# Kernel optimization log

Hardware: AMD Instinct MI355X
Metric: run time of the kernel (lower is better)

Reference implementation:

```python
import jax, jax.numpy as jnp
import numpy as np

VOCAB = 32000
D_MODEL = 192
N_LAYERS = 8
D_STATE = 64
EXPAND = 2
D_CONV = 3
NUM_CLASSES = 2
D_INNER = EXPAND * D_MODEL            # 384
DT_RANK = (D_MODEL + 15) // 16        # 12 (mamba_ssm default ceil(d_model/16))
EPS = 1e-6


def rmsnorm(x, w):
    return w * x * jax.lax.rsqrt(jnp.mean(x * x, axis=-1, keepdims=True) + EPS)


def selective_scan(u, dt, A, Bm, Cm):
    # u, dt: (b, T, d_inner); Bm, Cm: (b, T, d_state); A: (d_inner, d_state)
    def step(h, xs):
        dt_t, B_t, C_t, u_t = xs                      # (b,di),(b,ds),(b,ds),(b,di)
        dA = jnp.exp(dt_t[:, :, None] * A)            # (b, di, ds)
        h = dA * h + (dt_t * u_t)[:, :, None] * B_t[:, None, :]
        y = jnp.einsum('bdn,bn->bd', h, C_t)
        return h, y

    b = u.shape[0]
    h0 = jnp.zeros((b, D_INNER, D_STATE), u.dtype)
    xs = (jnp.swapaxes(dt, 0, 1), jnp.swapaxes(Bm, 0, 1),
          jnp.swapaxes(Cm, 0, 1), jnp.swapaxes(u, 0, 1))
    _, ys = jax.lax.scan(step, h0, xs)                # ys: (T, b, di)
    return jnp.swapaxes(ys, 0, 1)


def mamba_layer(x, p):
    # one residual Mamba block: x + Mamba(RMSNorm(x))
    norm_w, in_w, cw, cb, xpw, dtw, dtb, Alog, Dp, ow = p
    h = rmsnorm(x, norm_w)
    xz = jnp.einsum('btd,ed->bte', h, in_w)           # (b, T, 2*di)
    xi, z = jnp.split(xz, 2, axis=-1)
    # causal depthwise conv over time
    xc = jnp.swapaxes(xi, 1, 2)                       # (b, di, T)
    xc = jax.lax.conv_general_dilated(xc, cw[:, None, :], (1,),
                                      [(D_CONV - 1, 0)],
                                      feature_group_count=D_INNER)
    xi = jax.nn.silu(jnp.swapaxes(xc, 1, 2) + cb)
    dbl = jnp.einsum('btc,ec->bte', xi, xpw)          # (b, T, dt_rank+2*ds)
    dt_r = dbl[..., :DT_RANK]
    Bm = dbl[..., DT_RANK:DT_RANK + D_STATE]
    Cm = dbl[..., DT_RANK + D_STATE:]
    dt = jax.nn.softplus(jnp.einsum('btr,dr->btd', dt_r, dtw) + dtb)
    A = -jnp.exp(Alog)
    y = selective_scan(xi, dt, A, Bm, Cm) + xi * Dp
    y = y * jax.nn.silu(z)
    return x + jnp.einsum('bte,de->btd', y, ow)


def setup_inputs():
    key = jax.random.key(0)
    ks = jax.random.split(key, 12)
    B, L = 8, 1024
    s = 0.02
    input_ids = jax.random.randint(ks[0], (B, L), 0, VOCAB, dtype=jnp.int32)
    attention_mask = jnp.ones((B, L), dtype=jnp.int32)
    embed = jax.random.normal(ks[1], (VOCAB, D_MODEL), jnp.float32) * s
    cls = jax.random.normal(ks[2], (1, 1, D_MODEL), jnp.float32) * s
    norm_w = jnp.ones((N_LAYERS, D_MODEL), jnp.float32)
    in_proj_w = jax.random.normal(ks[3], (N_LAYERS, 2 * D_INNER, D_MODEL), jnp.float32) * s
    conv_w = jax.random.normal(ks[4], (N_LAYERS, D_INNER, D_CONV), jnp.float32) * s
    conv_b = jnp.zeros((N_LAYERS, D_INNER), jnp.float32)
    x_proj_w = jax.random.normal(ks[5], (N_LAYERS, DT_RANK + 2 * D_STATE, D_INNER), jnp.float32) * s
    dt_proj_w = jax.random.normal(ks[6], (N_LAYERS, D_INNER, DT_RANK), jnp.float32) * s
    dt_proj_b = jnp.zeros((N_LAYERS, D_INNER), jnp.float32)
    # mamba_ssm S4D-real init: A_log = log(1..d_state)
    A_log = jnp.log(jnp.tile(jnp.arange(1.0, D_STATE + 1, dtype=jnp.float32)[None, None, :],
                             (N_LAYERS, D_INNER, 1)))
    D_param = jnp.ones((N_LAYERS, D_INNER), jnp.float32)
    out_proj_w = jax.random.normal(ks[7], (N_LAYERS, D_MODEL, D_INNER), jnp.float32) * s
    final_norm_w = jnp.ones((D_MODEL,), jnp.float32)
    head_w = embed[:NUM_CLASSES]            # tie_embeddings=True
    head_b = jnp.zeros((NUM_CLASSES,), jnp.float32)
    return dict(input_ids=input_ids, attention_mask=attention_mask, embed=embed,
                cls=cls, norm_w=norm_w, in_proj_w=in_proj_w, conv_w=conv_w,
                conv_b=conv_b, x_proj_w=x_proj_w, dt_proj_w=dt_proj_w,
                dt_proj_b=dt_proj_b, A_log=A_log, D_param=D_param,
                out_proj_w=out_proj_w, final_norm_w=final_norm_w,
                head_w=head_w, head_b=head_b)


def reference(input_ids, attention_mask, embed, cls, norm_w, in_proj_w, conv_w,
              conv_b, x_proj_w, dt_proj_w, dt_proj_b, A_log, D_param,
              out_proj_w, final_norm_w, head_w, head_b):
    x = embed[input_ids]                               # (b, L, d)
    b = x.shape[0]
    x = jnp.concatenate([x, jnp.broadcast_to(cls, (b, 1, D_MODEL))], axis=1)
    layer_fn = jax.checkpoint(mamba_layer)

    def body(x, p):
        return layer_fn(x, p), None

    x, _ = jax.lax.scan(body, x, (norm_w, in_proj_w, conv_w, conv_b, x_proj_w,
                                  dt_proj_w, dt_proj_b, A_log, D_param, out_proj_w))
    x = rmsnorm(x, final_norm_w)
    m = attention_mask.astype(x.dtype)                 # (b, L)
    denom = jnp.clip(jnp.sum(m, axis=1, keepdims=True), 1.0, None)
    pooled = jnp.sum(x[:, :-1] * m[..., None], axis=1) / denom
    return pooled @ head_w.T + head_b                  # (b, num_classes)
```

## Files before the change

### kernel.cpp

```cpp
#include <hip/hip_runtime.h>
#include <hip/hip_bf16.h>
#include <cstddef>

namespace {

constexpr int NB   = 8;
constexpr int LSEQ = 1025;
constexpr int TSEQ = 1024;
constexpr int DM   = 192;
constexpr int DI   = 384;
constexpr int DXZ  = 768;
constexpr int DBLW = 140;
constexpr int DTR  = 12;
constexpr int NST  = 64;
constexpr int MROWS = NB * LSEQ;
constexpr int NCH  = 64;
constexpr int CS   = 16;
constexpr int NCH1 = NCH - 1;
constexpr int NDG  = DI / 64;
constexpr int HST  = 32;
constexpr int XPAD = 144;
constexpr float LOG2E = 1.4426950408889634f;

using bf16x8 = __attribute__((ext_vector_type(8))) short;
using f32x4  = __attribute__((ext_vector_type(4))) float;

__device__ __forceinline__ float waveReduceSum(float v) {
#pragma unroll
  for (int o = 32; o; o >>= 1) v += __shfl_xor(v, o, 64);
  return v;
}

__device__ __forceinline__ unsigned short f2bf(float v) {
  __hip_bfloat16 b = __float2bfloat16(v);
  return *reinterpret_cast<unsigned short*>(&b);
}
__device__ __forceinline__ float bf2f(unsigned short u) {
  return __uint_as_float(((unsigned)u) << 16);
}
__device__ __forceinline__ unsigned addpair_bf(unsigned a, unsigned b) {
  float alo = __uint_as_float(a << 16), ahi = __uint_as_float(a & 0xffff0000u);
  float blo = __uint_as_float(b << 16), bhi = __uint_as_float(b & 0xffff0000u);
  return ((unsigned)f2bf(alo + blo)) | (((unsigned)f2bf(ahi + bhi)) << 16);
}

__global__ void embed_kernel(const int* __restrict__ ids, const float* __restrict__ emb,
                             const float* __restrict__ cls, float* __restrict__ x) {
  int idx = blockIdx.x * blockDim.x + threadIdx.x;
  if (idx >= NB * LSEQ * DM) return;
  int d = idx % DM;
  int bt = idx / DM;
  int t = bt % LSEQ, b = bt / LSEQ;
  float v;
  if (t < TSEQ) v = emb[(size_t)ids[b * TSEQ + t] * DM + d];
  else          v = cls[d];
  x[idx] = v;
}

__global__ void cvt_bf16_kernel(const float* __restrict__ src, unsigned short* __restrict__ dst,
                                int n) {
  int idx = blockIdx.x * blockDim.x + threadIdx.x;
  if (idx < n) dst[idx] = f2bf(src[idx]);
}

__global__ void pad_xp_kernel(const float* __restrict__ src, unsigned short* __restrict__ dst) {
  int idx = blockIdx.x * blockDim.x + threadIdx.x;
  if (idx >= 8 * XPAD * DI) return;
  int k = idx % DI;
  int n = (idx / DI) % XPAD;
  int l = idx / (DI * XPAD);
  float v = (n < DBLW) ? src[((size_t)l * DBLW + n) * DI + k] : 0.f;
  dst[idx] = f2bf(v);
}

__global__ void transpose_batched(const float* __restrict__ in, float* __restrict__ out,
                                  int rows, int cols) {
  __shared__ float tile[32][33];
  int l = blockIdx.z;
  int r0 = blockIdx.y * 32, c0 = blockIdx.x * 32;
  const float* src = in + (size_t)l * rows * cols;
  float* dst = out + (size_t)l * rows * cols;
  int tx = threadIdx.x, ty = threadIdx.y;
#pragma unroll
  for (int i = 0; i < 32; i += 8) {
    int r = r0 + ty + i, c = c0 + tx;
    if (r < rows && c < cols) tile[ty + i][tx] = src[(size_t)r * cols + c];
  }
  __syncthreads();
#pragma unroll
  for (int i = 0; i < 32; i += 8) {
    int c = c0 + ty + i, r = r0 + tx;
    if (c < cols && r < rows) dst[(size_t)c * rows + r] = tile[tx][ty + i];
  }
}

__global__ __launch_bounds__(192)
void rmsnorm_kernel(const float* __restrict__ x, const float* __restrict__ w,
                    unsigned short* __restrict__ h) {
  int row = blockIdx.x;
  int d = threadIdx.x;
  float v = x[(size_t)row * DM + d];
  float ss = waveReduceSum(v * v);
  __shared__ float red[3];
  if ((d & 63) == 0) red[d >> 6] = ss;
  __syncthreads();
  float ms = (red[0] + red[1] + red[2]) * (1.f / DM);
  h[(size_t)row * DM + d] = f2bf(v * rsqrtf(ms + 1e-6f) * w[d]);
}

template <int EPI, int ASRC>
__global__ __launch_bounds__(256)
void gemm_mfma(const unsigned short* __restrict__ A, const unsigned short* __restrict__ Ab0,
               const unsigned short* __restrict__ Ab1, const unsigned short* __restrict__ W,
               float* __restrict__ C, unsigned short* __restrict__ Cb,
               int M, int Nw, int Nstore, int K, int ldc) {
  __shared__ unsigned short Alds[128][40];
  __shared__ unsigned short Wlds[64][40];
  const int tid = threadIdx.x;
  const int w = tid >> 6, lane = tid & 63;
  const int r16 = lane & 15, g = lane >> 4;
  const int row0 = blockIdx.y * 128, col0 = blockIdx.x * 64;

  f32x4 acc[2][4];
#pragma unroll
  for (int mi = 0; mi < 2; ++mi)
#pragma unroll
    for (int ni = 0; ni < 4; ++ni) acc[mi][ni] = (f32x4){0.f, 0.f, 0.f, 0.f};

  for (int k0 = 0; k0 < K; k0 += 32) {
#pragma unroll
    for (int cc = 0; cc < 2; ++cc) {
      int c = tid + cc * 256;
      int r = c >> 2, q = c & 3;
      uint4 v = make_uint4(0, 0, 0, 0);
      int grow = row0 + r;
      if (grow < M) {
        if (ASRC == 0) {
          v = *(const uint4*)(A + (size_t)grow * K + k0 + q * 8);
        } else {
          uint4 a = *(const uint4*)(Ab0 + (size_t)grow * K + k0 + q * 8);
          uint4 b = *(const uint4*)(Ab1 + (size_t)grow * K + k0 + q * 8);
          v.x = addpair_bf(a.x, b.x);
          v.y = addpair_bf(a.y, b.y);
          v.z = addpair_bf(a.z, b.z);
          v.w = addpair_bf(a.w, b.w);
        }
      }
      *(uint4*)&Alds[r][q * 8] = v;
    }
    {
      int r = tid >> 2, q = tid & 3;
      uint4 v = make_uint4(0, 0, 0, 0);
      int gn = col0 + r;
      if (gn < Nw) v = *(const uint4*)(W + (size_t)gn * K + k0 + q * 8);
      *(uint4*)&Wlds[r][q * 8] = v;
    }
    __syncthreads();
    bf16x8 a_f[2], b_f[4];
#pragma unroll
    for (int mi = 0; mi < 2; ++mi)
      a_f[mi] = *(const bf16x8*)&Alds[w * 32 + mi * 16 + r16][g * 8];
#pragma unroll
    for (int ni = 0; ni < 4; ++ni)
      b_f[ni] = *(const bf16x8*)&Wlds[ni * 16 + r16][g * 8];
#pragma unroll
    for (int mi = 0; mi < 2; ++mi)
#pragma unroll
      for (int ni = 0; ni < 4; ++ni)
        acc[mi][ni] = __builtin_amdgcn_mfma_f32_16x16x32_bf16(a_f[mi], b_f[ni],
                                                              acc[mi][ni], 0, 0, 0);
    __syncthreads();
  }
#pragma unroll
  for (int mi = 0; mi < 2; ++mi) {
#pragma unroll
    for (int reg = 0; reg < 4; ++reg) {
      int row = row0 + w * 32 + mi * 16 + g * 4 + reg;
      if (row >= M) continue;
#pragma unroll
      for (int ni = 0; ni < 4; ++ni) {
        int col = col0 + ni * 16 + r16;
        if (col >= Nstore) continue;
        size_t idx = (size_t)row * ldc + col;
        if (EPI == 1)      C[idx] += acc[mi][ni][reg];
        else if (EPI == 0) C[idx] = acc[mi][ni][reg];
        else               Cb[idx] = f2bf(acc[mi][ni][reg]);
      }
    }
  }
}

__global__ void conv_kernel(const unsigned short* __restrict__ xz16, const float* __restrict__ cw,
                            const float* __restrict__ cb,
                            unsigned short* __restrict__ xi16,
                            unsigned short* __restrict__ zg16) {
  int idx = blockIdx.x * blockDim.x + threadIdx.x;
  if (idx >= NB * LSEQ * DI) return;
  int c = idx % DI;
  int bt = idx / DI;
  int t = bt % LSEQ, b = bt / LSEQ;
  const unsigned short* src = xz16 + (size_t)b * LSEQ * DXZ + c;
  float s = cb[c];
  float w0 = cw[c * 3 + 0], w1 = cw[c * 3 + 1], w2 = cw[c * 3 + 2];
  if (t >= 2) s = fmaf(w0, bf2f(src[(size_t)(t - 2) * DXZ]), s);
  if (t >= 1) s = fmaf(w1, bf2f(src[(size_t)(t - 1) * DXZ]), s);
  s = fmaf(w2, bf2f(src[(size_t)t * DXZ]), s);
  float sig = 1.f / (1.f + __expf(-s));
  float u = s * sig;
  xi16[idx] = f2bf(u);
  float zv = bf2f(src[(size_t)t * DXZ + DI]);
  float zsig = 1.f / (1.f + __expf(-zv));
  zg16[idx] = f2bf(zv * zsig);
}

__global__ __launch_bounds__(384)
void dt_kernel(const float* __restrict__ dbl, const float* __restrict__ dtwT,
               const float* __restrict__ dtb, float* __restrict__ dtout) {
  int row0 = blockIdx.x * 4;
  int d = threadIdx.x;
  __shared__ float rr[4][DTR];
  if (d < 4 * DTR) rr[d / DTR][d % DTR] = dbl[(size_t)(row0 + d / DTR) * DBLW + (d % DTR)];
  float w[DTR];
#pragma unroll
  for (int r = 0; r < DTR; ++r) w[r] = dtwT[r * DI + d];
  float bias = dtb[d];
  __syncthreads();
#pragma unroll
  for (int q = 0; q < 4; ++q) {
    float s = bias;
#pragma unroll
    for (int r = 0; r < DTR; ++r) s = fmaf(rr[q][r], w[r], s);
    float sp = fmaxf(s, 0.f) + log1pf(__expf(-fabsf(s)));
    dtout[(size_t)(row0 + q) * DI + d] = sp;
  }
}


__global__ __launch_bounds__(768, 6)
void scan_pass1(const float* __restrict__ dtp_, const unsigned short* __restrict__ xi16,
                const float* __restrict__ dbl, const float* __restrict__ Alog,
                float* __restrict__ cumdt, float* __restrict__ H) {
  __shared__ float Bt[CS][64];
  const int tid = threadIdx.x;
  const int w = tid >> 6, lane = tid & 63;
  const int dgrp = w >> 1, half = w & 1;
  const int b = blockIdx.x / NCH1;
  const int c = blockIdx.x % NCH1;
  const int bg = b * NDG + dgrp;
  const int d = dgrp * 64 + lane;
  const int n0 = half * HST;
  const int t0 = c * CS;

  {
    const float* srcB = dbl + ((size_t)b * LSEQ + t0) * DBLW + DTR + lane;
    for (int r = w; r < CS; r += 12) Bt[r][lane] = srcB[(size_t)r * DBLW];
  }

  const float* Ap = Alog + (size_t)d * NST;
  float a0 = __expf(Ap[0]);
  bool okl = true;
#pragma unroll
  for (int j = 0; j < HST; ++j) {
    float aj = __expf(Ap[n0 + j]);
    okl = okl && (fabsf(aj - (float)(n0 + j + 1) * a0) <= 1e-3f * (float)(n0 + j + 1) * fabsf(a0));
  }
  const bool fast = __all(okl);
  const float al2u = -a0 * LOG2E;

  float h[HST];
#pragma unroll
  for (int j = 0; j < HST; ++j) h[j] = 0.f;

  __syncthreads();

  const float* dtp = dtp_ + ((size_t)b * LSEQ + t0) * DI + d;
  const unsigned short* up = xi16 + ((size_t)b * LSEQ + t0) * DI + d;
  float cum = 0.f;
  float dtv = *dtp, uv = bf2f(*up);

  if (fast) {
    for (int t = 0; t < CS; ++t) {
      float n_dt = 0.f, n_u = 0.f;
      if (t + 1 < CS) {
        dtp += DI; up += DI;
        n_dt = *dtp; n_u = bf2f(*up);
      }
      float dtu = dtv * uv;
      float m = dtv * al2u;
      float r1 = exp2f(m);
      float p = (n0 == 0) ? r1 : exp2f(m * (float)(n0 + 1));
      float r2 = r1 * r1, r4 = r2 * r2;
      float s0 = p, s1 = p * r1, s2 = p * r2, s3 = s2 * r1;
#pragma unroll
      for (int k = 0; k < 8; ++k) {
        float4 B4 = *(const float4*)&Bt[t][n0 + 4 * k];
        h[4 * k + 0] = fmaf(s0, h[4 * k + 0], dtu * B4.x);
        h[4 * k + 1] = fmaf(s1, h[4 * k + 1], dtu * B4.y);
        h[4 * k + 2] = fmaf(s2, h[4 * k + 2], dtu * B4.z);
        h[4 * k + 3] = fmaf(s3, h[4 * k + 3], dtu * B4.w);
        if (k < 7) { s0 *= r4; s1 *= r4; s2 *= r4; s3 *= r4; }
      }
      cum += dtv;
      dtv = n_dt; uv = n_u;
    }
  } else {
    for (int t = 0; t < CS; ++t) {
      float n_dt = 0.f, n_u = 0.f;
      if (t + 1 < CS) {
        dtp += DI; up += DI;
        n_dt = *dtp; n_u = bf2f(*up);
      }
      float dtu = dtv * uv;
      for (int j = 0; j < HST; ++j) {
        float aj = -__expf(Ap[n0 + j]) * LOG2E;
        h[j] = fmaf(exp2f(dtv * aj), h[j], dtu * Bt[t][n0 + j]);
      }
      cum += dtv;
      dtv = n_dt; uv = n_u;
    }
  }

  if (half == 0)
    cumdt[(size_t)bg * NCH1 * 64 + (size_t)c * 64 + lane] = cum;
  float* hp = H + ((size_t)bg * NCH + (c + 1)) * NST * 64 + (size_t)n0 * 64 + lane;
#pragma unroll
  for (int j = 0; j < HST; ++j) hp[j * 64] = h[j];
}

__global__ __launch_bounds__(256)
void scan_pass2(const float* __restrict__ cumdt, const float* __restrict__ Alog,
                float* __restrict__ H) {
  int gw = blockIdx.x * 4 + (threadIdx.x >> 6);
  int lane = threadIdx.x & 63;
  int bg = gw >> 4;
  int nq = (gw & 15) * 4;
  int dgrp = bg % NDG;
  int d = dgrp * 64 + lane;

  float al2[4];
#pragma unroll
  for (int j = 0; j < 4; ++j) al2[j] = -__expf(Alog[(size_t)d * NST + nq + j]) * LOG2E;

  float h[4] = {0.f, 0.f, 0.f, 0.f};

  float* H0 = H + ((size_t)bg * NCH) * NST * 64 + (size_t)nq * 64 + lane;
#pragma unroll
  for (int j = 0; j < 4; ++j) H0[j * 64] = 0.f;

  for (int c = 1; c < NCH; ++c) {
    float cum = cumdt[(size_t)bg * NCH1 * 64 + (size_t)(c - 1) * 64 + lane];
    float* Hc = H + ((size_t)bg * NCH + c) * NST * 64 + (size_t)nq * 64 + lane;
#pragma unroll
    for (int j = 0; j < 4; ++j) {
      float he = Hc[j * 64];
      h[j] = fmaf(exp2f(al2[j] * cum), h[j], he);
      Hc[j * 64] = h[j];
    }
  }
}

__global__ __launch_bounds__(768, 6)
void scan_pass3(const float* __restrict__ dtp_, const unsigned short* __restrict__ xi16,
                const unsigned short* __restrict__ zg16, const float* __restrict__ dbl,
                const float* __restrict__ Alog, const float* __restrict__ Dpar,
                const float* __restrict__ H, unsigned short* __restrict__ yb0,
                unsigned short* __restrict__ yb1) {
  __shared__ float Bt[CS + 1][64];
  __shared__ float Ct[CS + 1][64];
  const int tid = threadIdx.x;
  const int w = tid >> 6, lane = tid & 63;
  const int dgrp = w >> 1, half = w & 1;
  const int b = blockIdx.x >> 6;
  const int c = blockIdx.x & 63;
  const int bg = b * NDG + dgrp;
  const int d = dgrp * 64 + lane;
  const int n0 = half * HST;
  const int t0 = c * CS;
  const int nsteps = (c == NCH - 1) ? (LSEQ - t0) : CS;

  {
    if (w < 6) {
      const float* srcB = dbl + ((size_t)b * LSEQ + t0) * DBLW + DTR + lane;
      for (int r = w; r < nsteps; r += 6) Bt[r][lane] = srcB[(size_t)r * DBLW];
    } else {
      const float* srcC = dbl + ((size_t)b * LSEQ + t0) * DBLW + DTR + NST + lane;
      for (int r = w - 6; r < nsteps; r += 6) Ct[r][lane] = srcC[(size_t)r * DBLW];
    }
  }

  const float* Ap = Alog + (size_t)d * NST;
  float a0 = __expf(Ap[0]);
  bool okl = true;
#pragma unroll
  for (int j = 0; j < HST; ++j) {
    float aj = __expf(Ap[n0 + j]);
    okl = okl && (fabsf(aj - (float)(n0 + j + 1) * a0) <= 1e-3f * (float)(n0 + j + 1) * fabsf(a0));
  }
  const bool fast = __all(okl);
  const float al2u = -a0 * LOG2E;

  float Dp = Dpar[d];
  float h[HST];
  {
    const float* hi = H + ((size_t)bg * NCH + c) * NST * 64 + (size_t)n0 * 64 + lane;
#pragma unroll
    for (int j = 0; j < HST; ++j) h[j] = hi[j * 64];
  }

  __syncthreads();

  const float* dtp = dtp_ + ((size_t)b * LSEQ + t0) * DI + d;
  const unsigned short* up = xi16 + ((size_t)b * LSEQ + t0) * DI + d;
  const unsigned short* gp = zg16 + ((size_t)b * LSEQ + t0) * DI + d;
  unsigned short* yp = (half == 0 ? yb0 : yb1) + ((size_t)b * LSEQ + t0) * DI + d;

  float dtv = *dtp, uv = bf2f(*up), gv = bf2f(*gp);

  if (fast) {
    for (int t = 0; t < nsteps; ++t) {
      float n_dt = 0.f, n_u = 0.f, n_g = 0.f;
      if (t + 1 < nsteps) {
        dtp += DI; up += DI; gp += DI;
        n_dt = *dtp; n_u = bf2f(*up); n_g = bf2f(*gp);
      }
      float dtu = dtv * uv;
      float m = dtv * al2u;
      float r1 = exp2f(m);
      float p = (n0 == 0) ? r1 : exp2f(m * (float)(n0 + 1));
      float r2 = r1 * r1, r4 = r2 * r2;
      float s0 = p, s1 = p * r1, s2 = p * r2, s3 = s2 * r1;
      float y = 0.f;
#pragma unroll
      for (int k = 0; k < 8; ++k) {
        float4 B4 = *(const float4*)&Bt[t][n0 + 4 * k];
        float4 C4 = *(const float4*)&Ct[t][n0 + 4 * k];
        h[4 * k + 0] = fmaf(s0, h[4 * k + 0], dtu * B4.x);
        y = fmaf(h[4 * k + 0], C4.x, y);
        h[4 * k + 1] = fmaf(s1, h[4 * k + 1], dtu * B4.y);
        y = fmaf(h[4 * k + 1], C4.y, y);
        h[4 * k + 2] = fmaf(s2, h[4 * k + 2], dtu * B4.z);
        y = fmaf(h[4 * k + 2], C4.z, y);
        h[4 * k + 3] = fmaf(s3, h[4 * k + 3], dtu * B4.w);
        y = fmaf(h[4 * k + 3], C4.w, y);
        if (k < 7) { s0 *= r4; s1 *= r4; s2 *= r4; s3 *= r4; }
      }
      float outv = (half == 0) ? fmaf(uv, Dp, y) * gv : y * gv;
      *yp = f2bf(outv);
      yp += DI;
      dtv = n_dt; uv = n_u; gv = n_g;
    }
  } else {
    for (int t = 0; t < nsteps; ++t) {
      float n_dt = 0.f, n_u = 0.f, n_g = 0.f;
      if (t + 1 < nsteps) {
        dtp += DI; up += DI; gp += DI;
        n_dt = *dtp; n_u = bf2f(*up); n_g = bf2f(*gp);
      }
      float dtu = dtv * uv;
      float y = 0.f;
      for (int j = 0; j < HST; ++j) {
        float aj = -__expf(Ap[n0 + j]) * LOG2E;
        h[j] = fmaf(exp2f(dtv * aj), h[j], dtu * Bt[t][n0 + j]);
        y = fmaf(h[j], Ct[t][n0 + j], y);
      }
      float outv = (half == 0) ? fmaf(uv, Dp, y) * gv : y * gv;
      *yp = f2bf(outv);
      yp += DI;
      dtv = n_dt; uv = n_u; gv = n_g;
    }
  }
}

__global__ __launch_bounds__(192)
void pool1_kernel(const float* __restrict__ x, const int* __restrict__ mask,
                  const float* __restrict__ fw, float* __restrict__ partial) {
  int b = blockIdx.x >> 6;
  int chunk = blockIdx.x & 63;
  int d = threadIdx.x;
  __shared__ float red[3];
  float w = fw[d];
  float acc = 0.f;
  for (int tt = 0; tt < 16; ++tt) {
    int t = chunk * 16 + tt;
    float v = x[((size_t)b * LSEQ + t) * DM + d];
    float ss = waveReduceSum(v * v);
    if ((d & 63) == 0) red[d >> 6] = ss;
    __syncthreads();
    float ms = (red[0] + red[1] + red[2]) * (1.f / DM);
    float m = (float)mask[b * TSEQ + t];
    acc = fmaf(v * rsqrtf(ms + 1e-6f) * w, m, acc);
    __syncthreads();
  }
  partial[((size_t)b * 64 + chunk) * DM + d] = acc;
}

__global__ __launch_bounds__(192)
void pool2_kernel(const float* __restrict__ partial, const int* __restrict__ mask,
                  const float* __restrict__ hw, const float* __restrict__ hb,
                  float* __restrict__ out) {
  int b = blockIdx.x;
  int d = threadIdx.x;
  float s = 0.f;
  for (int c = 0; c < 64; ++c) s += partial[((size_t)b * 64 + c) * DM + d];
  float den = 0.f;
  for (int t = d; t < TSEQ; t += DM) den += (float)mask[b * TSEQ + t];
  den = waveReduceSum(den);
  __shared__ float dred[3];
  __shared__ float pooled[DM];
  if ((d & 63) == 0) dred[d >> 6] = den;
  __syncthreads();
  float denom = fmaxf(dred[0] + dred[1] + dred[2], 1.f);
  pooled[d] = s / denom;
  __syncthreads();
  if (d < 2) {
    float acc = hb[d];
    for (int k = 0; k < DM; ++k) acc = fmaf(pooled[k], hw[d * DM + k], acc);
    out[b * 2 + d] = acc;
  }
}

}

extern "C" void kernel_launch(void* const* d_in, const int* in_sizes, int n_in,
                              void* d_out, int out_size, void* d_ws, size_t ws_size,
                              hipStream_t stream) {
  const int*   ids    = (const int*)d_in[0];
  const int*   mask   = (const int*)d_in[1];
  const float* embed  = (const float*)d_in[2];
  const float* cls    = (const float*)d_in[3];
  const float* norm_w = (const float*)d_in[4];
  const float* in_w   = (const float*)d_in[5];
  const float* conv_w = (const float*)d_in[6];
  const float* conv_b = (const float*)d_in[7];
  const float* xp_w   = (const float*)d_in[8];
  const float* dtw    = (const float*)d_in[9];
  const float* dtb    = (const float*)d_in[10];
  const float* Alog   = (const float*)d_in[11];
  const float* Dpar   = (const float*)d_in[12];
  const float* ow     = (const float*)d_in[13];
  const float* fnw    = (const float*)d_in[14];
  const float* hw     = (const float*)d_in[15];
  const float* hb     = (const float*)d_in[16];
  float* out = (float*)d_out;

  char* base = (char*)d_ws;
  size_t off = 0;
  auto alloc = [&](size_t bytes) -> void* {
    void* p = base + off;
    off = (off + bytes + 255) & ~(size_t)255;
    return p;
  };

  float* x      = (float*)alloc((size_t)NB * LSEQ * DM * 4);
  unsigned short* h16 = (unsigned short*)alloc((size_t)NB * LSEQ * DM * 2);
  unsigned short* xz16 = (unsigned short*)alloc((size_t)NB * LSEQ * DXZ * 2);
  unsigned short* xi16 = (unsigned short*)alloc((size_t)NB * LSEQ * DI * 2);
  unsigned short* zg16 = (unsigned short*)alloc((size_t)NB * LSEQ * DI * 2);
  float* dblb   = (float*)alloc((size_t)NB * LSEQ * DBLW * 4);
  float* dtbuf  = (float*)alloc((size_t)NB * LSEQ * DI * 4);
  unsigned short* yb0 = (unsigned short*)alloc((size_t)NB * LSEQ * DI * 2);
  unsigned short* yb1 = (unsigned short*)alloc((size_t)NB * LSEQ * DI * 2);
  unsigned short* wb_in = (unsigned short*)alloc((size_t)8 * DXZ * DM * 2);
  unsigned short* wb_xp = (unsigned short*)alloc((size_t)8 * XPAD * DI * 2);
  unsigned short* wb_ow = (unsigned short*)alloc((size_t)8 * DM * DI * 2);
  float* wT_dt  = (float*)alloc((size_t)8 * DTR * DI * 4);
  float* partial = (float*)alloc((size_t)NB * 64 * DM * 4);
  float* cumdt  = (float*)alloc((size_t)NB * NDG * NCH1 * 64 * 4);
  float* Hbuf   = (float*)alloc((size_t)NB * NDG * NCH * NST * 64 * 4);

  cvt_bf16_kernel<<<(8 * DXZ * DM + 255) / 256, 256, 0, stream>>>(in_w, wb_in, 8 * DXZ * DM);
  pad_xp_kernel<<<(8 * XPAD * DI + 255) / 256, 256, 0, stream>>>(xp_w, wb_xp);
  cvt_bf16_kernel<<<(8 * DM * DI + 255) / 256, 256, 0, stream>>>(ow, wb_ow, 8 * DM * DI);
  dim3 tb(32, 8);
  transpose_batched<<<dim3(1, 12, 8), tb, 0, stream>>>(dtw, wT_dt, DI, DTR);

  embed_kernel<<<(NB * LSEQ * DM) / 256, 256, 0, stream>>>(ids, embed, cls, x);

  const int mtiles = (MROWS + 127) / 128;
  for (int l = 0; l < 8; ++l) {
    rmsnorm_kernel<<<MROWS, 192, 0, stream>>>(x, norm_w + l * DM, h16);
    gemm_mfma<2, 0><<<dim3(DXZ / 64, mtiles), 256, 0, stream>>>(
        h16, nullptr, nullptr, wb_in + (size_t)l * DXZ * DM, nullptr, xz16,
        MROWS, DXZ, DXZ, DM, DXZ);
    conv_kernel<<<(NB * LSEQ * DI) / 256, 256, 0, stream>>>(
        xz16, conv_w + l * DI * 3, conv_b + l * DI, xi16, zg16);
    gemm_mfma<0, 0><<<dim3(XPAD / 64 + 1, mtiles), 256, 0, stream>>>(
        xi16, nullptr, nullptr, wb_xp + (size_t)l * XPAD * DI, dblb, nullptr,
        MROWS, XPAD, DBLW, DI, DBLW);
    dt_kernel<<<MROWS / 4, DI, 0, stream>>>(dblb, wT_dt + l * DTR * DI, dtb + l * DI, dtbuf);
    scan_pass1<<<NB * NCH1, 768, 0, stream>>>(
        dtbuf, xi16, dblb, Alog + (size_t)l * DI * NST, cumdt, Hbuf);
    scan_pass2<<<(NB * NDG * 16) / 4, 256, 0, stream>>>(
        cumdt, Alog + (size_t)l * DI * NST, Hbuf);
    scan_pass3<<<NB * NCH, 768, 0, stream>>>(
        dtbuf, xi16, zg16, dblb, Alog + (size_t)l * DI * NST, Dpar + l * DI, Hbuf,
        yb0, yb1);
    gemm_mfma<1, 1><<<dim3(DM / 64, mtiles), 256, 0, stream>>>(
        nullptr, yb0, yb1, wb_ow + (size_t)l * DM * DI, x, nullptr,
        MROWS, DM, DM, DI, DM);
  }

  pool1_kernel<<<NB * 64, 192, 0, stream>>>(x, mask, fnw, partial);
  pool2_kernel<<<NB, 192, 0, stream>>>(partial, mask, hw, hb, out);
}
```

Baseline: 1.391 ms.

## Split scan state into quarters with longer chunks and four partial-y buffers

Changes the chunked selective scan from 64 chunks of 16 steps with two state-halves per d-group to 32 chunks of 32 steps. Each wave now owns a quarter of the state (16 registers), and each block covers half of the d-groups. Four partial y buffers are written and then summed inside the out-projection GEMM's A-load. The aim is lower register pressure per thread and less inter-chunk H traffic in pass2, with more parallel lanes per step. The cost is extra y-buffer memory traffic, four loads per A element in the GEMM, and longer serial chunks.

```diff
diff --git a/kernel.cpp b/kernel.cpp
--- a/kernel.cpp
+++ b/kernel.cpp
@@ -14,11 +14,11 @@
 constexpr int DTR  = 12;
 constexpr int NST  = 64;
 constexpr int MROWS = NB * LSEQ;
-constexpr int NCH  = 64;
-constexpr int CS   = 16;
+constexpr int NCH  = 32;
+constexpr int CS   = 32;
 constexpr int NCH1 = NCH - 1;
 constexpr int NDG  = DI / 64;
-constexpr int HST  = 32;
+constexpr int HST  = 16;
 constexpr int XPAD = 144;
 constexpr float LOG2E = 1.4426950408889634f;
 
@@ -111,7 +111,8 @@
 template <int EPI, int ASRC>
 __global__ __launch_bounds__(256)
 void gemm_mfma(const unsigned short* __restrict__ A, const unsigned short* __restrict__ Ab0,
-               const unsigned short* __restrict__ Ab1, const unsigned short* __restrict__ W,
+               const unsigned short* __restrict__ Ab1, const unsigned short* __restrict__ Ab2,
+               const unsigned short* __restrict__ Ab3, const unsigned short* __restrict__ W,
                float* __restrict__ C, unsigned short* __restrict__ Cb,
                int M, int Nw, int Nstore, int K, int ldc) {
   __shared__ unsigned short Alds[128][40];
@@ -140,10 +141,12 @@
         } else {
           uint4 a = *(const uint4*)(Ab0 + (size_t)grow * K + k0 + q * 8);
           uint4 b = *(const uint4*)(Ab1 + (size_t)grow * K + k0 + q * 8);
-          v.x = addpair_bf(a.x, b.x);
-          v.y = addpair_bf(a.y, b.y);
-          v.z = addpair_bf(a.z, b.z);
-          v.w = addpair_bf(a.w, b.w);
+          uint4 cq = *(const uint4*)(Ab2 + (size_t)grow * K + k0 + q * 8);
+          uint4 dq = *(const uint4*)(Ab3 + (size_t)grow * K + k0 + q * 8);
+          v.x = addpair_bf(addpair_bf(a.x, b.x), addpair_bf(cq.x, dq.x));
+          v.y = addpair_bf(addpair_bf(a.y, b.y), addpair_bf(cq.y, dq.y));
+          v.z = addpair_bf(addpair_bf(a.z, b.z), addpair_bf(cq.z, dq.z));
+          v.w = addpair_bf(addpair_bf(a.w, b.w), addpair_bf(cq.w, dq.w));
         }
       }
       *(uint4*)&Alds[r][q * 8] = v;
@@ -243,12 +246,14 @@
   __shared__ float Bt[CS][64];
   const int tid = threadIdx.x;
   const int w = tid >> 6, lane = tid & 63;
-  const int dgrp = w >> 1, half = w & 1;
-  const int b = blockIdx.x / NCH1;
-  const int c = blockIdx.x % NCH1;
+  const int dgrp_l = w >> 2, quarter = w & 3;
+  const int b = blockIdx.x / (NCH1 * 2);
+  const int rem = blockIdx.x % (NCH1 * 2);
+  const int c = rem >> 1, hb = rem & 1;
+  const int dgrp = hb * 3 + dgrp_l;
   const int bg = b * NDG + dgrp;
   const int d = dgrp * 64 + lane;
-  const int n0 = half * HST;
+  const int n0 = quarter * HST;
   const int t0 = c * CS;
 
   {
@@ -288,17 +293,17 @@
       float dtu = dtv * uv;
       float m = dtv * al2u;
       float r1 = exp2f(m);
-      float p = (n0 == 0) ? r1 : exp2f(m * (float)(n0 + 1));
+      float p = (quarter == 0) ? r1 : exp2f(m * (float)(n0 + 1));
       float r2 = r1 * r1, r4 = r2 * r2;
       float s0 = p, s1 = p * r1, s2 = p * r2, s3 = s2 * r1;
 #pragma unroll
-      for (int k = 0; k < 8; ++k) {
+      for (int k = 0; k < HST / 4; ++k) {
         float4 B4 = *(const float4*)&Bt[t][n0 + 4 * k];
         h[4 * k + 0] = fmaf(s0, h[4 * k + 0], dtu * B4.x);
         h[4 * k + 1] = fmaf(s1, h[4 * k + 1], dtu * B4.y);
         h[4 * k + 2] = fmaf(s2, h[4 * k + 2], dtu * B4.z);
         h[4 * k + 3] = fmaf(s3, h[4 * k + 3], dtu * B4.w);
-        if (k < 7) { s0 *= r4; s1 *= r4; s2 *= r4; s3 *= r4; }
+        if (k < HST / 4 - 1) { s0 *= r4; s1 *= r4; s2 *= r4; s3 *= r4; }
       }
       cum += dtv;
       dtv = n_dt; uv = n_u;
@@ -320,7 +325,7 @@
     }
   }
 
-  if (half == 0)
+  if (quarter == 0)
     cumdt[(size_t)bg * NCH1 * 64 + (size_t)c * 64 + lane] = cum;
   float* hp = H + ((size_t)bg * NCH + (c + 1)) * NST * 64 + (size_t)n0 * 64 + lane;
 #pragma unroll
@@ -363,18 +368,21 @@
 void scan_pass3(const float* __restrict__ dtp_, const unsigned short* __restrict__ xi16,
                 const unsigned short* __restrict__ zg16, const float* __restrict__ dbl,
                 const float* __restrict__ Alog, const float* __restrict__ Dpar,
-                const float* __restrict__ H, unsigned short* __restrict__ yb0,
-                unsigned short* __restrict__ yb1) {
+                const float* __restrict__ H,
+                unsigned short* __restrict__ yq0, unsigned short* __restrict__ yq1,
+                unsigned short* __restrict__ yq2, unsigned short* __restrict__ yq3) {
   __shared__ float Bt[CS + 1][64];
   __shared__ float Ct[CS + 1][64];
   const int tid = threadIdx.x;
   const int w = tid >> 6, lane = tid & 63;
-  const int dgrp = w >> 1, half = w & 1;
+  const int dgrp_l = w >> 2, quarter = w & 3;
   const int b = blockIdx.x >> 6;
-  const int c = blockIdx.x & 63;
+  const int rem = blockIdx.x & 63;
+  const int c = rem >> 1, hb = rem & 1;
+  const int dgrp = hb * 3 + dgrp_l;
   const int bg = b * NDG + dgrp;
   const int d = dgrp * 64 + lane;
-  const int n0 = half * HST;
+  const int n0 = quarter * HST;
   const int t0 = c * CS;
   const int nsteps = (c == NCH - 1) ? (LSEQ - t0) : CS;
 
@@ -412,7 +420,8 @@
   const float* dtp = dtp_ + ((size_t)b * LSEQ + t0) * DI + d;
   const unsigned short* up = xi16 + ((size_t)b * LSEQ + t0) * DI + d;
   const unsigned short* gp = zg16 + ((size_t)b * LSEQ + t0) * DI + d;
-  unsigned short* yp = (half == 0 ? yb0 : yb1) + ((size_t)b * LSEQ + t0) * DI + d;
+  unsigned short* yp = (quarter == 0 ? yq0 : quarter == 1 ? yq1 : quarter == 2 ? yq2 : yq3)
+                       + ((size_t)b * LSEQ + t0) * DI + d;
 
   float dtv = *dtp, uv = bf2f(*up), gv = bf2f(*gp);
 
@@ -426,12 +435,12 @@
       float dtu = dtv * uv;
       float m = dtv * al2u;
       float r1 = exp2f(m);
-      float p = (n0 == 0) ? r1 : exp2f(m * (float)(n0 + 1));
+      float p = (quarter == 0) ? r1 : exp2f(m * (float)(n0 + 1));
       float r2 = r1 * r1, r4 = r2 * r2;
       float s0 = p, s1 = p * r1, s2 = p * r2, s3 = s2 * r1;
       float y = 0.f;
 #pragma unroll
-      for (int k = 0; k < 8; ++k) {
+      for (int k = 0; k < HST / 4; ++k) {
         float4 B4 = *(const float4*)&Bt[t][n0 + 4 * k];
         float4 C4 = *(const float4*)&Ct[t][n0 + 4 * k];
         h[4 * k + 0] = fmaf(s0, h[4 * k + 0], dtu * B4.x);
@@ -442,9 +451,9 @@
         y = fmaf(h[4 * k + 2], C4.z, y);
         h[4 * k + 3] = fmaf(s3, h[4 * k + 3], dtu * B4.w);
         y = fmaf(h[4 * k + 3], C4.w, y);
-        if (k < 7) { s0 *= r4; s1 *= r4; s2 *= r4; s3 *= r4; }
-      }
-      float outv = (half == 0) ? fmaf(uv, Dp, y) * gv : y * gv;
+        if (k < HST / 4 - 1) { s0 *= r4; s1 *= r4; s2 *= r4; s3 *= r4; }
+      }
+      float outv = (quarter == 0) ? fmaf(uv, Dp, y) * gv : y * gv;
       *yp = f2bf(outv);
       yp += DI;
       dtv = n_dt; uv = n_u; gv = n_g;
@@ -463,7 +472,7 @@
         h[j] = fmaf(exp2f(dtv * aj), h[j], dtu * Bt[t][n0 + j]);
         y = fmaf(h[j], Ct[t][n0 + j], y);
       }
-      float outv = (half == 0) ? fmaf(uv, Dp, y) * gv : y * gv;
+      float outv = (quarter == 0) ? fmaf(uv, Dp, y) * gv : y * gv;
       *yp = f2bf(outv);
       yp += DI;
       dtv = n_dt; uv = n_u; gv = n_g;
@@ -558,8 +567,10 @@
   unsigned short* zg16 = (unsigned short*)alloc((size_t)NB * LSEQ * DI * 2);
   float* dblb   = (float*)alloc((size_t)NB * LSEQ * DBLW * 4);
   float* dtbuf  = (float*)alloc((size_t)NB * LSEQ * DI * 4);
-  unsigned short* yb0 = (unsigned short*)alloc((size_t)NB * LSEQ * DI * 2);
-  unsigned short* yb1 = (unsigned short*)alloc((size_t)NB * LSEQ * DI * 2);
+  unsigned short* yq0 = (unsigned short*)alloc((size_t)NB * LSEQ * DI * 2);
+  unsigned short* yq1 = (unsigned short*)alloc((size_t)NB * LSEQ * DI * 2);
+  unsigned short* yq2 = (unsigned short*)alloc((size_t)NB * LSEQ * DI * 2);
+  unsigned short* yq3 = (unsigned short*)alloc((size_t)NB * LSEQ * DI * 2);
   unsigned short* wb_in = (unsigned short*)alloc((size_t)8 * DXZ * DM * 2);
   unsigned short* wb_xp = (unsigned short*)alloc((size_t)8 * XPAD * DI * 2);
   unsigned short* wb_ow = (unsigned short*)alloc((size_t)8 * DM * DI * 2);
@@ -580,24 +591,24 @@
   for (int l = 0; l < 8; ++l) {
     rmsnorm_kernel<<<MROWS, 192, 0, stream>>>(x, norm_w + l * DM, h16);
     gemm_mfma<2, 0><<<dim3(DXZ / 64, mtiles), 256, 0, stream>>>(
-        h16, nullptr, nullptr, wb_in + (size_t)l * DXZ * DM, nullptr, xz16,
-        MROWS, DXZ, DXZ, DM, DXZ);
+        h16, nullptr, nullptr, nullptr, nullptr, wb_in + (size_t)l * DXZ * DM,
+        nullptr, xz16, MROWS, DXZ, DXZ, DM, DXZ);
     conv_kernel<<<(NB * LSEQ * DI) / 256, 256, 0, stream>>>(
         xz16, conv_w + l * DI * 3, conv_b + l * DI, xi16, zg16);
     gemm_mfma<0, 0><<<dim3(XPAD / 64 + 1, mtiles), 256, 0, stream>>>(
-        xi16, nullptr, nullptr, wb_xp + (size_t)l * XPAD * DI, dblb, nullptr,
-        MROWS, XPAD, DBLW, DI, DBLW);
+        xi16, nullptr, nullptr, nullptr, nullptr, wb_xp + (size_t)l * XPAD * DI,
+        dblb, nullptr, MROWS, XPAD, DBLW, DI, DBLW);
     dt_kernel<<<MROWS / 4, DI, 0, stream>>>(dblb, wT_dt + l * DTR * DI, dtb + l * DI, dtbuf);
-    scan_pass1<<<NB * NCH1, 768, 0, stream>>>(
+    scan_pass1<<<NB * NCH1 * 2, 768, 0, stream>>>(
         dtbuf, xi16, dblb, Alog + (size_t)l * DI * NST, cumdt, Hbuf);
     scan_pass2<<<(NB * NDG * 16) / 4, 256, 0, stream>>>(
         cumdt, Alog + (size_t)l * DI * NST, Hbuf);
-    scan_pass3<<<NB * NCH, 768, 0, stream>>>(
+    scan_pass3<<<NB * NCH * 2, 768, 0, stream>>>(
         dtbuf, xi16, zg16, dblb, Alog + (size_t)l * DI * NST, Dpar + l * DI, Hbuf,
-        yb0, yb1);
+        yq0, yq1, yq2, yq3);
     gemm_mfma<1, 1><<<dim3(DM / 64, mtiles), 256, 0, stream>>>(
-        nullptr, yb0, yb1, wb_ow + (size_t)l * DM * DI, x, nullptr,
-        MROWS, DM, DM, DI, DM);
+        nullptr, yq0, yq1, yq2, yq3, wb_ow + (size_t)l * DM * DI,
+        x, nullptr, MROWS, DM, DM, DI, DM);
   }
 
   pool1_kernel<<<NB * 64, 192, 0, stream>>>(x, mask, fnw, partial);
```

After: 1.319 ms. -5.1%, faster.

## Restructure chunked scan: scalar B/C loads, bf16 chunk states, larger chunks

Applied to the files above, without the earlier changes.

The chunked selective scan now uses 32-step chunks instead of 16, which halves the number of chunk states. Blocks shrink from 768 to 128 threads, each handling one 64-channel group. B and C are no longer staged in shared memory; they are read through wave-uniform (readfirstlane) pointers so they can go through scalar loads, which also removes the __syncthreads. Inter-chunk states H are stored in bf16 instead of fp32 to halve that traffic, and the y reduction is split into four accumulators for more ILP. The bf16 state storage loses precision across the chunk carry, and longer chunks lengthen the serial part of each block.

```diff
diff --git a/kernel.cpp b/kernel.cpp
--- a/kernel.cpp
+++ b/kernel.cpp
@@ -14,8 +14,8 @@
 constexpr int DTR  = 12;
 constexpr int NST  = 64;
 constexpr int MROWS = NB * LSEQ;
-constexpr int NCH  = 64;
-constexpr int CS   = 16;
+constexpr int NCH  = 32;
+constexpr int CS   = 32;
 constexpr int NCH1 = NCH - 1;
 constexpr int NDG  = DI / 64;
 constexpr int HST  = 32;
@@ -42,6 +42,12 @@
   float alo = __uint_as_float(a << 16), ahi = __uint_as_float(a & 0xffff0000u);
   float blo = __uint_as_float(b << 16), bhi = __uint_as_float(b & 0xffff0000u);
   return ((unsigned)f2bf(alo + blo)) | (((unsigned)f2bf(ahi + bhi)) << 16);
+}
+__device__ __forceinline__ const float* uniform_ptr(const float* p) {
+  unsigned long long v = (unsigned long long)p;
+  unsigned lo = __builtin_amdgcn_readfirstlane((unsigned)v);
+  unsigned hi = __builtin_amdgcn_readfirstlane((unsigned)(v >> 32));
+  return (const float*)(((unsigned long long)hi << 32) | lo);
 }
 
 __global__ void embed_kernel(const int* __restrict__ ids, const float* __restrict__ emb,
@@ -236,25 +242,23 @@
 }
 
 
-__global__ __launch_bounds__(768, 6)
+__global__ __launch_bounds__(128, 4)
 void scan_pass1(const float* __restrict__ dtp_, const unsigned short* __restrict__ xi16,
                 const float* __restrict__ dbl, const float* __restrict__ Alog,
-                float* __restrict__ cumdt, float* __restrict__ H) {
-  __shared__ float Bt[CS][64];
+                float* __restrict__ cumdt, unsigned short* __restrict__ H) {
   const int tid = threadIdx.x;
-  const int w = tid >> 6, lane = tid & 63;
-  const int dgrp = w >> 1, half = w & 1;
-  const int b = blockIdx.x / NCH1;
-  const int c = blockIdx.x % NCH1;
+  const int half = tid >> 6, lane = tid & 63;
+  const int b = blockIdx.x / (NCH1 * NDG);
+  const int rem = blockIdx.x % (NCH1 * NDG);
+  const int c = rem / NDG;
+  const int dgrp = rem % NDG;
   const int bg = b * NDG + dgrp;
   const int d = dgrp * 64 + lane;
   const int n0 = half * HST;
   const int t0 = c * CS;
 
-  {
-    const float* srcB = dbl + ((size_t)b * LSEQ + t0) * DBLW + DTR + lane;
-    for (int r = w; r < CS; r += 12) Bt[r][lane] = srcB[(size_t)r * DBLW];
-  }
+  const int n0u = __builtin_amdgcn_readfirstlane(n0);
+  const float* Bg = uniform_ptr(dbl + ((size_t)b * LSEQ + t0) * DBLW + DTR + n0u);
 
   const float* Ap = Alog + (size_t)d * NST;
   float a0 = __expf(Ap[0]);
@@ -270,8 +274,6 @@
   float h[HST];
 #pragma unroll
   for (int j = 0; j < HST; ++j) h[j] = 0.f;
-
-  __syncthreads();
 
   const float* dtp = dtp_ + ((size_t)b * LSEQ + t0) * DI + d;
   const unsigned short* up = xi16 + ((size_t)b * LSEQ + t0) * DI + d;
@@ -288,12 +290,13 @@
       float dtu = dtv * uv;
       float m = dtv * al2u;
       float r1 = exp2f(m);
-      float p = (n0 == 0) ? r1 : exp2f(m * (float)(n0 + 1));
+      float p = (n0u == 0) ? r1 : exp2f(m * (float)(n0u + 1));
       float r2 = r1 * r1, r4 = r2 * r2;
       float s0 = p, s1 = p * r1, s2 = p * r2, s3 = s2 * r1;
+      const float* Bu = Bg + (size_t)t * DBLW;
 #pragma unroll
       for (int k = 0; k < 8; ++k) {
-        float4 B4 = *(const float4*)&Bt[t][n0 + 4 * k];
+        float4 B4 = *(const float4*)(Bu + 4 * k);
         h[4 * k + 0] = fmaf(s0, h[4 * k + 0], dtu * B4.x);
         h[4 * k + 1] = fmaf(s1, h[4 * k + 1], dtu * B4.y);
         h[4 * k + 2] = fmaf(s2, h[4 * k + 2], dtu * B4.z);
@@ -311,9 +314,10 @@
         n_dt = *dtp; n_u = bf2f(*up);
       }
       float dtu = dtv * uv;
+      const float* Bu = Bg + (size_t)t * DBLW;
       for (int j = 0; j < HST; ++j) {
         float aj = -__expf(Ap[n0 + j]) * LOG2E;
-        h[j] = fmaf(exp2f(dtv * aj), h[j], dtu * Bt[t][n0 + j]);
+        h[j] = fmaf(exp2f(dtv * aj), h[j], dtu * Bu[j]);
       }
       cum += dtv;
       dtv = n_dt; uv = n_u;
@@ -322,14 +326,14 @@
 
   if (half == 0)
     cumdt[(size_t)bg * NCH1 * 64 + (size_t)c * 64 + lane] = cum;
-  float* hp = H + ((size_t)bg * NCH + (c + 1)) * NST * 64 + (size_t)n0 * 64 + lane;
-#pragma unroll
-  for (int j = 0; j < HST; ++j) hp[j * 64] = h[j];
+  unsigned short* hp = H + ((size_t)bg * NCH + (c + 1)) * NST * 64 + (size_t)n0 * 64 + lane;
+#pragma unroll
+  for (int j = 0; j < HST; ++j) hp[j * 64] = f2bf(h[j]);
 }
 
 __global__ __launch_bounds__(256)
 void scan_pass2(const float* __restrict__ cumdt, const float* __restrict__ Alog,
-                float* __restrict__ H) {
+                unsigned short* __restrict__ H) {
   int gw = blockIdx.x * 4 + (threadIdx.x >> 6);
   int lane = threadIdx.x & 63;
   int bg = gw >> 4;
@@ -343,50 +347,43 @@
 
   float h[4] = {0.f, 0.f, 0.f, 0.f};
 
-  float* H0 = H + ((size_t)bg * NCH) * NST * 64 + (size_t)nq * 64 + lane;
-#pragma unroll
-  for (int j = 0; j < 4; ++j) H0[j * 64] = 0.f;
+  unsigned short* H0 = H + ((size_t)bg * NCH) * NST * 64 + (size_t)nq * 64 + lane;
+#pragma unroll
+  for (int j = 0; j < 4; ++j) H0[j * 64] = 0;
 
   for (int c = 1; c < NCH; ++c) {
     float cum = cumdt[(size_t)bg * NCH1 * 64 + (size_t)(c - 1) * 64 + lane];
-    float* Hc = H + ((size_t)bg * NCH + c) * NST * 64 + (size_t)nq * 64 + lane;
+    unsigned short* Hc = H + ((size_t)bg * NCH + c) * NST * 64 + (size_t)nq * 64 + lane;
 #pragma unroll
     for (int j = 0; j < 4; ++j) {
-      float he = Hc[j * 64];
+      float he = bf2f(Hc[j * 64]);
       h[j] = fmaf(exp2f(al2[j] * cum), h[j], he);
-      Hc[j * 64] = h[j];
-    }
-  }
-}
-
-__global__ __launch_bounds__(768, 6)
+      Hc[j * 64] = f2bf(h[j]);
+    }
+  }
+}
+
+__global__ __launch_bounds__(128, 4)
 void scan_pass3(const float* __restrict__ dtp_, const unsigned short* __restrict__ xi16,
                 const unsigned short* __restrict__ zg16, const float* __restrict__ dbl,
                 const float* __restrict__ Alog, const float* __restrict__ Dpar,
-                const float* __restrict__ H, unsigned short* __restrict__ yb0,
+                const unsigned short* __restrict__ H, unsigned short* __restrict__ yb0,
                 unsigned short* __restrict__ yb1) {
-  __shared__ float Bt[CS + 1][64];
-  __shared__ float Ct[CS + 1][64];
   const int tid = threadIdx.x;
-  const int w = tid >> 6, lane = tid & 63;
-  const int dgrp = w >> 1, half = w & 1;
-  const int b = blockIdx.x >> 6;
-  const int c = blockIdx.x & 63;
+  const int half = tid >> 6, lane = tid & 63;
+  const int b = blockIdx.x / (NCH * NDG);
+  const int rem = blockIdx.x % (NCH * NDG);
+  const int c = rem / NDG;
+  const int dgrp = rem % NDG;
   const int bg = b * NDG + dgrp;
   const int d = dgrp * 64 + lane;
   const int n0 = half * HST;
   const int t0 = c * CS;
   const int nsteps = (c == NCH - 1) ? (LSEQ - t0) : CS;
 
-  {
-    if (w < 6) {
-      const float* srcB = dbl + ((size_t)b * LSEQ + t0) * DBLW + DTR + lane;
-      for (int r = w; r < nsteps; r += 6) Bt[r][lane] = srcB[(size_t)r * DBLW];
-    } else {
-      const float* srcC = dbl + ((size_t)b * LSEQ + t0) * DBLW + DTR + NST + lane;
-      for (int r = w - 6; r < nsteps; r += 6) Ct[r][lane] = srcC[(size_t)r * DBLW];
-    }
-  }
+  const int n0u = __builtin_amdgcn_readfirstlane(n0);
+  const float* Bg = uniform_ptr(dbl + ((size_t)b * LSEQ + t0) * DBLW + DTR + n0u);
+  const float* Cg = Bg + NST;
 
   const float* Ap = Alog + (size_t)d * NST;
   float a0 = __expf(Ap[0]);
@@ -402,12 +399,10 @@
   float Dp = Dpar[d];
   float h[HST];
   {
-    const float* hi = H + ((size_t)bg * NCH + c) * NST * 64 + (size_t)n0 * 64 + lane;
-#pragma unroll
-    for (int j = 0; j < HST; ++j) h[j] = hi[j * 64];
-  }
-
-  __syncthreads();
+    const unsigned short* hi = H + ((size_t)bg * NCH + c) * NST * 64 + (size_t)n0 * 64 + lane;
+#pragma unroll
+    for (int j = 0; j < HST; ++j) h[j] = bf2f(hi[j * 64]);
+  }
 
   const float* dtp = dtp_ + ((size_t)b * LSEQ + t0) * DI + d;
   const unsigned short* up = xi16 + ((size_t)b * LSEQ + t0) * DI + d;
@@ -426,24 +421,27 @@
       float dtu = dtv * uv;
       float m = dtv * al2u;
       float r1 = exp2f(m);
-      float p = (n0 == 0) ? r1 : exp2f(m * (float)(n0 + 1));
+      float p = (n0u == 0) ? r1 : exp2f(m * (float)(n0u + 1));
       float r2 = r1 * r1, r4 = r2 * r2;
       float s0 = p, s1 = p * r1, s2 = p * r2, s3 = s2 * r1;
-      float y = 0.f;
+      float y0 = 0.f, y1 = 0.f, y2 = 0.f, y3 = 0.f;
+      const float* Bu = Bg + (size_t)t * DBLW;
+      const float* Cu = Cg + (size_t)t * DBLW;
 #pragma unroll
       for (int k = 0; k < 8; ++k) {
-        float4 B4 = *(const float4*)&Bt[t][n0 + 4 * k];
-        float4 C4 = *(const float4*)&Ct[t][n0 + 4 * k];
+        float4 B4 = *(const float4*)(Bu + 4 * k);
+        float4 C4 = *(const float4*)(Cu + 4 * k);
         h[4 * k + 0] = fmaf(s0, h[4 * k + 0], dtu * B4.x);
-        y = fmaf(h[4 * k + 0], C4.x, y);
+        y0 = fmaf(h[4 * k + 0], C4.x, y0);
         h[4 * k + 1] = fmaf(s1, h[4 * k + 1], dtu * B4.y);
-        y = fmaf(h[4 * k + 1], C4.y, y);
+        y1 = fmaf(h[4 * k + 1], C4.y, y1);
         h[4 * k + 2] = fmaf(s2, h[4 * k + 2], dtu * B4.z);
-        y = fmaf(h[4 * k + 2], C4.z, y);
+        y2 = fmaf(h[4 * k + 2], C4.z, y2);
         h[4 * k + 3] = fmaf(s3, h[4 * k + 3], dtu * B4.w);
-        y = fmaf(h[4 * k + 3], C4.w, y);
+        y3 = fmaf(h[4 * k + 3], C4.w, y3);
         if (k < 7) { s0 *= r4; s1 *= r4; s2 *= r4; s3 *= r4; }
       }
+      float y = (y0 + y1) + (y2 + y3);
       float outv = (half == 0) ? fmaf(uv, Dp, y) * gv : y * gv;
       *yp = f2bf(outv);
       yp += DI;
@@ -458,10 +456,12 @@
       }
       float dtu = dtv * uv;
       float y = 0.f;
+      const float* Bu = Bg + (size_t)t * DBLW;
+      const float* Cu = Cg + (size_t)t * DBLW;
       for (int j = 0; j < HST; ++j) {
         float aj = -__expf(Ap[n0 + j]) * LOG2E;
-        h[j] = fmaf(exp2f(dtv * aj), h[j], dtu * Bt[t][n0 + j]);
-        y = fmaf(h[j], Ct[t][n0 + j], y);
+        h[j] = fmaf(exp2f(dtv * aj), h[j], dtu * Bu[j]);
+        y = fmaf(h[j], Cu[j], y);
       }
       float outv = (half == 0) ? fmaf(uv, Dp, y) * gv : y * gv;
       *yp = f2bf(outv);
@@ -566,7 +566,7 @@
   float* wT_dt  = (float*)alloc((size_t)8 * DTR * DI * 4);
   float* partial = (float*)alloc((size_t)NB * 64 * DM * 4);
   float* cumdt  = (float*)alloc((size_t)NB * NDG * NCH1 * 64 * 4);
-  float* Hbuf   = (float*)alloc((size_t)NB * NDG * NCH * NST * 64 * 4);
+  unsigned short* Hbuf = (unsigned short*)alloc((size_t)NB * NDG * NCH * NST * 64 * 2);
 
   cvt_bf16_kernel<<<(8 * DXZ * DM + 255) / 256, 256, 0, stream>>>(in_w, wb_in, 8 * DXZ * DM);
   pad_xp_kernel<<<(8 * XPAD * DI + 255) / 256, 256, 0, stream>>>(xp_w, wb_xp);
@@ -588,11 +588,11 @@
         xi16, nullptr, nullptr, wb_xp + (size_t)l * XPAD * DI, dblb, nullptr,
         MROWS, XPAD, DBLW, DI, DBLW);
     dt_kernel<<<MROWS / 4, DI, 0, stream>>>(dblb, wT_dt + l * DTR * DI, dtb + l * DI, dtbuf);
-    scan_pass1<<<NB * NCH1, 768, 0, stream>>>(
+    scan_pass1<<<NB * NCH1 * NDG, 128, 0, stream>>>(
         dtbuf, xi16, dblb, Alog + (size_t)l * DI * NST, cumdt, Hbuf);
     scan_pass2<<<(NB * NDG * 16) / 4, 256, 0, stream>>>(
         cumdt, Alog + (size_t)l * DI * NST, Hbuf);
-    scan_pass3<<<NB * NCH, 768, 0, stream>>>(
+    scan_pass3<<<NB * NCH * NDG, 128, 0, stream>>>(
         dtbuf, xi16, zg16, dblb, Alog + (size_t)l * DI * NST, Dpar + l * DI, Hbuf,
         yb0, yb1);
     gemm_mfma<1, 1><<<dim3(DM / 64, mtiles), 256, 0, stream>>>(
```

Measured after the change: 1.866 ms. 1.34x slower.
